# Kernel tuning notes

Measured on AMD Instinct MI355X. Metric: run time of the kernel, lower is better.

## Reference

```python
import jax, jax.numpy as jnp
import numpy as np

N_NODES = 10000
AVG_DEG = 16
N_EDGES = N_NODES * AVG_DEG
NODE_DIM, EDGE_DIM, LIN_DIM, HID, OUT, LAYERS = 9, 3, 32, 300, 2, 5


def _init(key, shape, fan_in):
    return jax.random.normal(key, shape, jnp.float32) * (1.0 / np.sqrt(fan_in))


def setup_inputs() -> dict:
    key = jax.random.key(0)
    ks = jax.random.split(key, 18)
    inp = {
        "x": jax.random.normal(ks[0], (N_NODES, NODE_DIM), jnp.float32),
        "edge_index": jax.random.randint(ks[1], (2, N_EDGES), 0, N_NODES, jnp.int32),
        "edge_attr": jax.random.normal(ks[2], (N_EDGES, EDGE_DIM), jnp.float32),
        "batch": jnp.zeros((N_NODES,), jnp.int32),
        # nn.Linear params (stored as [in, out] so fwd is x @ W + b)
        "node_w": _init(ks[3], (NODE_DIM, LIN_DIM), NODE_DIM),
        "node_b": jnp.zeros((LIN_DIM,), jnp.float32),
        "edge_w": _init(ks[4], (EDGE_DIM, LIN_DIM), EDGE_DIM),
        "edge_b": jnp.zeros((LIN_DIM,), jnp.float32),
        # GCNConv: lin (no bias) + separate additive bias (PyG convention)
        "gcn0_w": _init(ks[5], (LIN_DIM, HID), LIN_DIM),
        "gcn0_b": jnp.zeros((HID,), jnp.float32),
        "gcn_w": _init(ks[6], (LAYERS - 1, HID, HID), HID),
        "gcn_b": jnp.zeros((LAYERS - 1, HID), jnp.float32),
        "lin1_w": _init(ks[7], (HID, LIN_DIM), HID),
        "lin1_b": jnp.zeros((LIN_DIM,), jnp.float32),
        "lin2_w": _init(ks[8], (LIN_DIM, OUT), LIN_DIM),
        "lin2_b": jnp.zeros((OUT,), jnp.float32),
    }
    return inp


def reference(x, edge_index, edge_attr, batch,
              node_w, node_b, edge_w, edge_b,
              gcn0_w, gcn0_b, gcn_w, gcn_b,
              lin1_w, lin1_b, lin2_w, lin2_b):
    row, col = edge_index[0], edge_index[1]

    e = edge_attr @ edge_w + edge_b  # [E, LIN_DIM] edge embeddings

    # Faithful to the original bug: node embeddings get edge attrs scatter-added,
    # then the result is discarded by `attr = edge_attr`. Kept for fidelity (dead).
    node_h = x @ node_w + node_b
    node_h = node_h.at[row].add(e)  # unused downstream

    # GCN stack runs over the E-row edge-embedding matrix -> effective node count = E
    h = e
    n = h.shape[0]  # == N_EDGES

    # symmetric gcn_norm with self-loops (edge_weight = 1), computed once
    deg = jax.ops.segment_sum(jnp.ones((edge_index.shape[1],), h.dtype), col,
                              num_segments=n) + 1.0
    dinv = jax.lax.rsqrt(deg)
    norm = dinv[row] * dinv[col]  # per-edge normalization
    self_norm = (dinv * dinv)[:, None]  # self-loop term

    def gcn(h, w, b):
        hw = h @ w  # dense transform
        agg = jax.ops.segment_sum(hw[row] * norm[:, None], col, num_segments=n)
        return agg + self_norm * hw + b

    h = jax.nn.relu(gcn(h, gcn0_w, gcn0_b))

    def step(h, wb):
        w, b = wb
        return jax.nn.relu(gcn(h, w, b)), None

    h, _ = jax.lax.scan(step, h, (gcn_w, gcn_b))

    g = jnp.mean(h, axis=0, keepdims=True)  # [1, HID] graph readout
    g = jax.nn.relu(g @ lin1_w + lin1_b)
    pred = g @ lin2_w + lin2_b  # [1, OUT]; forward returns pre-softmax logits
    return pred
```

## Files before the change

kernel.cpp:

```cpp
#include <hip/hip_runtime.h>
#include <hip/hip_bf16.h>

#define N_NODES 10000
#define N_EDGES 160000
#define HID 300
#define HIDP 304
#define NPARTB (N_EDGES - N_NODES)
#define KS 328
#define RBM 80
#define RBF 32
#define PARTB_BLOCKS 1875
#define GEMMA_BLOCKS 125
#define FILL_BLOCKS 313
#define MEGA_BLOCKS (PARTB_BLOCKS + GEMMA_BLOCKS + FILL_BLOCKS)
#define FUSE_BLOCKS 313

typedef __attribute__((ext_vector_type(8))) short short8;
typedef __attribute__((ext_vector_type(4))) float f32x4;

#define MFMA_B16(a, b, c) __builtin_amdgcn_mfma_f32_16x16x32_bf16(a, b, c, 0, 0, 0)

__device__ __forceinline__ short bf16r(float x) {
    unsigned u = __float_as_uint(x);
    return (short)((u + 0x7fffu + ((u >> 16) & 1u)) >> 16);
}
__device__ __forceinline__ float b2f(unsigned short u) {
    return __uint_as_float(((unsigned)u) << 16);
}
__device__ __forceinline__ void split1(float x, short& hi, short& lo) {
    short h = bf16r(x);
    float hf = __uint_as_float(((unsigned)(unsigned short)h) << 16);
    hi = h;
    lo = bf16r(x - hf);
}

__global__ void k_prep(const float* __restrict__ g0w, const float* __restrict__ gw,
                       short* __restrict__ wt0, short* __restrict__ wtl,
                       const int* __restrict__ col, int* __restrict__ cnt) {
    int idx = blockIdx.x * 256 + threadIdx.x;
    if (idx < N_EDGES) atomicAdd(&cnt[col[idx]], 1);
    if (idx < 1216) {
        int n16 = idx & 15, q = (idx >> 4) & 3, nt = idx >> 6;
        int n = nt * 16 + n16;
        short* hd = wt0 + (size_t)(nt * 8 + q) * 128 + n16 * 8;
        short* ld = wt0 + (size_t)(nt * 8 + 4 + q) * 128 + n16 * 8;
#pragma unroll
        for (int j = 0; j < 8; ++j) {
            int k = q * 8 + j;
            float f = (n < HID) ? g0w[k * HID + n] : 0.0f;
            short hi, lo;
            split1(f, hi, lo);
            hd[j] = hi;
            ld[j] = lo;
        }
    } else if (idx < 1216 + 48640) {
        int i = idx - 1216;
        int n16 = i & 15; i >>= 4;
        int q = i & 3; i >>= 2;
        int nt = i % 19; i /= 19;
        int chunk = i % 10;
        int l = i / 10;
        int n = nt * 16 + n16;
        int cnt_idx = chunk * 19 + nt;
        short* base = wtl + (size_t)l * 194560;
        short* hd = base + (size_t)(cnt_idx * 8 + q) * 128 + n16 * 8;
        short* ld = base + (size_t)(cnt_idx * 8 + 4 + q) * 128 + n16 * 8;
#pragma unroll
        for (int j = 0; j < 8; ++j) {
            int k = chunk * 32 + q * 8 + j;
            float f = (k < HID && n < HID) ? gw[((size_t)l * HID + k) * HID + n] : 0.0f;
            short hi, lo;
            split1(f, hi, lo);
            hd[j] = hi;
            ld[j] = lo;
        }
    }
}

__global__ __launch_bounds__(1024) void k_scan(
    const int* __restrict__ cnt, int* __restrict__ col_start,
    int* __restrict__ cursor, float* __restrict__ dinv,
    float* __restrict__ selfnorm) {
    __shared__ int wsum[16];
    int t = threadIdx.x;
    int lane = t & 63, w = t >> 6;
    int carry = 0;
    for (int base = 0; base < N_NODES; base += 1024) {
        int i = base + t;
        int v = (i < N_NODES) ? cnt[i] : 0;
        int s = v;
#pragma unroll
        for (int d = 1; d < 64; d <<= 1) {
            int n = __shfl_up(s, d, 64);
            if (lane >= d) s += n;
        }
        if (lane == 63) wsum[w] = s;
        __syncthreads();
        int woff = 0, total = 0;
#pragma unroll
        for (int k = 0; k < 16; ++k) {
            if (k < w) woff += wsum[k];
            total += wsum[k];
        }
        if (i < N_NODES) {
            int excl = carry + woff + s - v;
            col_start[i] = excl;
            cursor[i] = excl;
            float dd = (float)v + 1.0f;
            dinv[i] = rsqrtf(dd);
            selfnorm[i] = 1.0f / dd;
        }
        carry += total;
        __syncthreads();
    }
    if (t == 0) col_start[N_NODES] = carry;
}

template <int MT, int NTC>
__device__ __forceinline__ void kloop(const short* __restrict__ wp, int nch,
                                      const short* Hh, int nt0, int quad, int l16,
                                      f32x4 (&acc)[MT][NTC]) {
#pragma unroll
    for (int mt = 0; mt < MT; ++mt)
#pragma unroll
        for (int i = 0; i < NTC; ++i)
#pragma unroll
            for (int r = 0; r < 4; ++r) acc[mt][i][r] = 0.0f;
#pragma unroll 1
    for (int c = 0; c < nch; ++c) {
        const short* cb = wp + (size_t)(c * 19 + nt0) * 1024 + quad * 128 + l16 * 8;
        short8 ah[MT];
#pragma unroll
        for (int mt = 0; mt < MT; ++mt)
            ah[mt] = *(const short8*)&Hh[(mt * 16 + l16) * KS + c * 32 + quad * 8];
        short8 bb[NTC];
#pragma unroll
        for (int i = 0; i < NTC; ++i) bb[i] = *(const short8*)(cb + (size_t)i * 1024);
#pragma unroll
        for (int mt = 0; mt < MT; ++mt)
#pragma unroll
            for (int i = 0; i < NTC; ++i)
                acc[mt][i] = MFMA_B16(ah[mt], bb[i], acc[mt][i]);
#pragma unroll
        for (int i = 0; i < NTC; ++i) bb[i] = *(const short8*)(cb + (size_t)i * 1024 + 512);
#pragma unroll
        for (int mt = 0; mt < MT; ++mt)
#pragma unroll
            for (int i = 0; i < NTC; ++i)
                acc[mt][i] = MFMA_B16(ah[mt], bb[i], acc[mt][i]);
    }
}

template <int MT, int NTC>
__device__ __forceinline__ void gcn_epilogue(const float* __restrict__ bias,
                                             int nt0, int quad, int l16,
                                             f32x4 (&acc)[MT][NTC], short* Hh) {
#pragma unroll
    for (int i = 0; i < NTC; ++i) {
        int c = (nt0 + i) * 16 + l16;
        float b = (c < HID) ? bias[c] : 0.0f;
#pragma unroll
        for (int mt = 0; mt < MT; ++mt)
#pragma unroll
            for (int r = 0; r < 4; ++r) {
                float v = fmaxf(acc[mt][i][r] + b, 0.0f);
                Hh[(mt * 16 + quad * 4 + r) * KS + c] = bf16r(v);
            }
    }
}

template <int MT, int NTC>
__device__ __forceinline__ void gcn_final(const float* __restrict__ bias,
                                          int nt0, int quad, int l16,
                                          f32x4 (&acc)[MT][NTC],
                                          float* __restrict__ gout) {
#pragma unroll
    for (int i = 0; i < NTC; ++i) {
        int c = (nt0 + i) * 16 + l16;
        float b = (c < HID) ? bias[c] : 0.0f;
        float s = 0.0f;
#pragma unroll
        for (int mt = 0; mt < MT; ++mt)
#pragma unroll
            for (int r = 0; r < 4; ++r) s += fmaxf(acc[mt][i][r] + b, 0.0f);
        s += __shfl_xor(s, 16, 64);
        s += __shfl_xor(s, 32, 64);
        if (quad == 0) gout[c] = (c < HID) ? s : 0.0f;
    }
}

template <int MT, int NTC>
__device__ __forceinline__ void gemm_out(int base, int nt0, int quad, int l16,
                                         f32x4 (&acc)[MT][NTC],
                                         unsigned short* __restrict__ HW) {
#pragma unroll
    for (int i = 0; i < NTC; ++i) {
        int c = (nt0 + i) * 16 + l16;
#pragma unroll
        for (int mt = 0; mt < MT; ++mt)
#pragma unroll
            for (int r = 0; r < 4; ++r) {
                int gm = base + mt * 16 + quad * 4 + r;
                if (gm < N_NODES)
                    HW[(size_t)gm * HIDP + c] = (unsigned short)bf16r(acc[mt][i][r]);
            }
    }
}

__global__ __launch_bounds__(512, 4) void k_mega(
    const float* __restrict__ edge_attr,
    const float* __restrict__ edge_w,
    const float* __restrict__ edge_b,
    const short* __restrict__ wt0,
    const short* __restrict__ wtl,
    const float* __restrict__ gcn0_b,
    const float* __restrict__ gcn_b,
    float* __restrict__ gpartB,
    unsigned short* __restrict__ hw0,
    const int* __restrict__ row,
    const int* __restrict__ col,
    int* __restrict__ cursor,
    const float* __restrict__ dinv,
    int2* __restrict__ edge_pack) {
    __shared__ short Hh[RBM * KS];
    int bid = blockIdx.x, t = threadIdx.x;
    int lane = t & 63, w = t >> 6;
    int l16 = lane & 15, quad = lane >> 4;
    int nt0 = (w < 3) ? w * 3 : 9 + (w - 3) * 2;

    if (bid < PARTB_BLOCKS) {
        int base = N_NODES + bid * RBM;
        for (int i = t; i < RBM * 8; i += 512) {
            int r = i >> 3, c4 = (i & 7) * 4;
            const float* ar = edge_attr + (size_t)(base + r) * 3;
            float a0 = ar[0], a1 = ar[1], a2 = ar[2];
#pragma unroll
            for (int j = 0; j < 4; ++j) {
                int cc = c4 + j;
                float v = edge_b[cc];
                v = fmaf(a0, edge_w[cc], v);
                v = fmaf(a1, edge_w[32 + cc], v);
                v = fmaf(a2, edge_w[64 + cc], v);
                Hh[r * KS + cc] = bf16r(v);
            }
        }
        for (int i = t; i < RBM * 24; i += 512) {
            int r = i / 24, k = 304 + i % 24;
            Hh[r * KS + k] = 0;
        }
        __syncthreads();

        float* gout = gpartB + (size_t)bid * HIDP;
        if (w < 3) {
            f32x4 acc[5][3];
            kloop<5, 3>(wt0, 1, Hh, nt0, quad, l16, acc);
            __syncthreads();
            gcn_epilogue<5, 3>(gcn0_b, nt0, quad, l16, acc, Hh);
            __syncthreads();
            for (int l = 0; l < 4; ++l) {
                kloop<5, 3>(wtl + (size_t)l * 194560, 10, Hh, nt0, quad, l16, acc);
                __syncthreads();
                if (l < 3) {
                    gcn_epilogue<5, 3>(gcn_b + l * HID, nt0, quad, l16, acc, Hh);
                    __syncthreads();
                } else {
                    gcn_final<5, 3>(gcn_b + l * HID, nt0, quad, l16, acc, gout);
                }
            }
        } else {
            f32x4 acc[5][2];
            kloop<5, 2>(wt0, 1, Hh, nt0, quad, l16, acc);
            __syncthreads();
            gcn_epilogue<5, 2>(gcn0_b, nt0, quad, l16, acc, Hh);
            __syncthreads();
            for (int l = 0; l < 4; ++l) {
                kloop<5, 2>(wtl + (size_t)l * 194560, 10, Hh, nt0, quad, l16, acc);
                __syncthreads();
                if (l < 3) {
                    gcn_epilogue<5, 2>(gcn_b + l * HID, nt0, quad, l16, acc, Hh);
                    __syncthreads();
                } else {
                    gcn_final<5, 2>(gcn_b + l * HID, nt0, quad, l16, acc, gout);
                }
            }
        }
    } else if (bid < PARTB_BLOCKS + GEMMA_BLOCKS) {
        int base = (bid - PARTB_BLOCKS) * RBM;
        for (int i = t; i < RBM * 8; i += 512) {
            int r = i >> 3, c4 = (i & 7) * 4;
            const float* ar = edge_attr + (size_t)(base + r) * 3;
            float a0 = ar[0], a1 = ar[1], a2 = ar[2];
#pragma unroll
            for (int j = 0; j < 4; ++j) {
                int cc = c4 + j;
                float v = edge_b[cc];
                v = fmaf(a0, edge_w[cc], v);
                v = fmaf(a1, edge_w[32 + cc], v);
                v = fmaf(a2, edge_w[64 + cc], v);
                Hh[r * KS + cc] = bf16r(v);
            }
        }
        for (int i = t; i < RBM * 24; i += 512) {
            int r = i / 24, k = 304 + i % 24;
            Hh[r * KS + k] = 0;
        }
        __syncthreads();
        if (w < 3) {
            f32x4 acc[5][3];
            kloop<5, 3>(wt0, 1, Hh, nt0, quad, l16, acc);
            gemm_out<5, 3>(base, nt0, quad, l16, acc, hw0);
        } else {
            f32x4 acc[5][2];
            kloop<5, 2>(wt0, 1, Hh, nt0, quad, l16, acc);
            gemm_out<5, 2>(base, nt0, quad, l16, acc, hw0);
        }
    } else {
        int e = (bid - PARTB_BLOCKS - GEMMA_BLOCKS) * 512 + t;
        if (e < N_EDGES) {
            int c = col[e], r = row[e];
            int p = atomicAdd(&cursor[c], 1);
            edge_pack[p] = make_int2(r, __float_as_int(dinv[r] * dinv[c]));
        }
    }
}

__device__ __forceinline__ void agg_row(int c, int lane,
                                        const unsigned short* __restrict__ hw_in,
                                        const int* __restrict__ col_start,
                                        const int2* __restrict__ edge_pack,
                                        float (&v)[5]) {
#pragma unroll
    for (int jj = 0; jj < 5; ++jj) v[jj] = 0.0f;
    int beg = col_start[c], end = col_start[c + 1];
    int i = beg;
    for (; i + 4 <= end; i += 4) {
        int2 e0 = edge_pack[i], e1 = edge_pack[i + 1];
        int2 e2 = edge_pack[i + 2], e3 = edge_pack[i + 3];
        const unsigned short* h0 = hw_in + (size_t)e0.x * HIDP;
        const unsigned short* h1 = hw_in + (size_t)e1.x * HIDP;
        const unsigned short* h2 = hw_in + (size_t)e2.x * HIDP;
        const unsigned short* h3 = hw_in + (size_t)e3.x * HIDP;
        float n0 = __int_as_float(e0.y), n1 = __int_as_float(e1.y);
        float n2 = __int_as_float(e2.y), n3 = __int_as_float(e3.y);
#pragma unroll
        for (int jj = 0; jj < 5; ++jj) {
            int cc = lane + 64 * jj;
            if (cc < HIDP) {
                float s = v[jj];
                s = fmaf(n0, b2f(h0[cc]), s);
                s = fmaf(n1, b2f(h1[cc]), s);
                s = fmaf(n2, b2f(h2[cc]), s);
                s = fmaf(n3, b2f(h3[cc]), s);
                v[jj] = s;
            }
        }
    }
    for (; i < end; ++i) {
        int2 e0 = edge_pack[i];
        const unsigned short* h0 = hw_in + (size_t)e0.x * HIDP;
        float n0 = __int_as_float(e0.y);
#pragma unroll
        for (int jj = 0; jj < 5; ++jj) {
            int cc = lane + 64 * jj;
            if (cc < HIDP) v[jj] = fmaf(n0, b2f(h0[cc]), v[jj]);
        }
    }
}

__global__ __launch_bounds__(512, 6) void k_fuse(
    const unsigned short* __restrict__ hw_in,
    const int* __restrict__ col_start,
    const int2* __restrict__ edge_pack,
    const float* __restrict__ selfnorm,
    const float* __restrict__ bias,
    const short* __restrict__ wt,
    unsigned short* __restrict__ hw_out) {
    __shared__ short Hh[RBF * KS];
    int t = threadIdx.x;
    int lane = t & 63, w = t >> 6;
    int l16 = lane & 15, quad = lane >> 4;
    int base = blockIdx.x * RBF;
    int nt0 = (w < 3) ? w * 3 : 9 + (w - 3) * 2;

#pragma unroll 1
    for (int j = 0; j < 4; ++j) {
        int r = w * 4 + j;
        int c = base + r;
        if (c < N_NODES) {
            float v[5];
            agg_row(c, lane, hw_in, col_start, edge_pack, v);
            float sn = selfnorm[c];
            const unsigned short* sp = hw_in + (size_t)c * HIDP;
#pragma unroll
            for (int jj = 0; jj < 5; ++jj) {
                int cc = lane + 64 * jj;
                if (cc < HIDP) {
                    float h = v[jj] + sn * b2f(sp[cc]) + ((cc < HID) ? bias[cc] : 0.0f);
                    Hh[r * KS + cc] = bf16r(fmaxf(h, 0.0f));
                }
            }
        } else {
#pragma unroll
            for (int jj = 0; jj < 5; ++jj) {
                int cc = lane + 64 * jj;
                if (cc < HIDP) Hh[r * KS + cc] = 0;
            }
        }
    }
    for (int i = t; i < RBF * 24; i += 512) {
        int r = i / 24, k = 304 + i % 24;
        Hh[r * KS + k] = 0;
    }
    __syncthreads();

    if (w < 3) {
        f32x4 acc[2][3];
        kloop<2, 3>(wt, 10, Hh, nt0, quad, l16, acc);
        gemm_out<2, 3>(base, nt0, quad, l16, acc, hw_out);
    } else {
        f32x4 acc[2][2];
        kloop<2, 2>(wt, 10, Hh, nt0, quad, l16, acc);
        gemm_out<2, 2>(base, nt0, quad, l16, acc, hw_out);
    }
}

__global__ __launch_bounds__(512) void k_last(
    const unsigned short* __restrict__ hw_in,
    const int* __restrict__ col_start,
    const int2* __restrict__ edge_pack,
    const float* __restrict__ selfnorm,
    const float* __restrict__ bias,
    const float* __restrict__ gpartB,
    float* __restrict__ g_sum) {
    __shared__ float red[8 * 320];
    int t = threadIdx.x;
    int lane = t & 63, w = t >> 6;
    int base = blockIdx.x * RBF;

    float s[5] = {0.0f, 0.0f, 0.0f, 0.0f, 0.0f};
#pragma unroll 1
    for (int j = 0; j < 4; ++j) {
        int c = base + w * 4 + j;
        if (c < N_NODES) {
            float v[5];
            agg_row(c, lane, hw_in, col_start, edge_pack, v);
            float sn = selfnorm[c];
            const unsigned short* sp = hw_in + (size_t)c * HIDP;
#pragma unroll
            for (int jj = 0; jj < 5; ++jj) {
                int cc = lane + 64 * jj;
                if (cc < HID) {
                    float h = v[jj] + sn * b2f(sp[cc]) + bias[cc];
                    s[jj] += fmaxf(h, 0.0f);
                }
            }
        }
    }
    if (w < 6) {
        int rr = blockIdx.x * 6 + w;
        if (rr < PARTB_BLOCKS) {
#pragma unroll
            for (int jj = 0; jj < 5; ++jj) {
                int cc = lane + 64 * jj;
                if (cc < HID) s[jj] += gpartB[(size_t)rr * HIDP + cc];
            }
        }
    }
#pragma unroll
    for (int jj = 0; jj < 5; ++jj) red[w * 320 + lane + 64 * jj] = s[jj];
    __syncthreads();
    if (w == 0) {
#pragma unroll
        for (int jj = 0; jj < 5; ++jj) {
            int cc = lane + 64 * jj;
            if (cc < HID) {
                float tot = 0.0f;
#pragma unroll
                for (int g = 0; g < 8; ++g) tot += red[g * 320 + cc];
                atomicAdd(&g_sum[cc], tot);
            }
        }
    }
}

__global__ void k_head(const float* __restrict__ g_sum,
                       const float* __restrict__ lin1_w, const float* __restrict__ lin1_b,
                       const float* __restrict__ lin2_w, const float* __restrict__ lin2_b,
                       float* __restrict__ out) {
    __shared__ float g2[32];
    int t = threadIdx.x;
    const float inv = 1.0f / (float)N_EDGES;
    if (t < 32) {
        float a = lin1_b[t];
        for (int d = 0; d < HID; ++d) a = fmaf(g_sum[d] * inv, lin1_w[d * 32 + t], a);
        g2[t] = fmaxf(a, 0.0f);
    }
    __syncthreads();
    if (t < 2) {
        float p = lin2_b[t];
        for (int j = 0; j < 32; ++j) p = fmaf(g2[j], lin2_w[j * 2 + t], p);
        out[t] = p;
    }
}


extern "C" void kernel_launch(void* const* d_in, const int* in_sizes, int n_in,
                              void* d_out, int out_size, void* d_ws, size_t ws_size,
                              hipStream_t stream) {
    (void)in_sizes; (void)n_in; (void)out_size; (void)ws_size;
    const int* edge_index = (const int*)d_in[1];
    const float* edge_attr = (const float*)d_in[2];
    const float* edge_w = (const float*)d_in[6];
    const float* edge_b = (const float*)d_in[7];
    const float* gcn0_w = (const float*)d_in[8];
    const float* gcn0_b = (const float*)d_in[9];
    const float* gcn_w = (const float*)d_in[10];
    const float* gcn_b = (const float*)d_in[11];
    const float* lin1_w = (const float*)d_in[12];
    const float* lin1_b = (const float*)d_in[13];
    const float* lin2_w = (const float*)d_in[14];
    const float* lin2_b = (const float*)d_in[15];

    char* ws = (char*)d_ws;
    size_t off = 0;
    auto alloc = [&](size_t bytes) {
        void* p = ws + off;
        off = (off + bytes + 255) & ~(size_t)255;
        return p;
    };
    unsigned short* hwA = (unsigned short*)alloc((size_t)N_NODES * HIDP * 2);
    unsigned short* hwB = (unsigned short*)alloc((size_t)N_NODES * HIDP * 2);
    int2* edge_pack = (int2*)alloc((size_t)N_EDGES * 8);
    int* cnt = (int*)alloc((size_t)N_NODES * 4);
    int* col_start = (int*)alloc((size_t)(N_NODES + 1) * 4);
    int* cursor = (int*)alloc((size_t)N_NODES * 4);
    float* dinv = (float*)alloc((size_t)N_NODES * 4);
    float* selfnorm = (float*)alloc((size_t)N_NODES * 4);
    float* g_sum = (float*)alloc((size_t)HIDP * 4);
    short* wt0 = (short*)alloc((size_t)38912);
    short* wtl = (short*)alloc((size_t)4 * 389120);
    float* gpartB = (float*)alloc((size_t)PARTB_BLOCKS * HIDP * 4);

    const int* row = edge_index;
    const int* col = edge_index + N_EDGES;

    hipMemsetAsync(cnt, 0, N_NODES * 4, stream);
    hipMemsetAsync(g_sum, 0, HIDP * 4, stream);

    k_prep<<<(N_EDGES + 255) / 256, 256, 0, stream>>>(gcn0_w, gcn_w, wt0, wtl, col, cnt);
    k_scan<<<1, 1024, 0, stream>>>(cnt, col_start, cursor, dinv, selfnorm);

    k_mega<<<MEGA_BLOCKS, 512, 0, stream>>>(edge_attr, edge_w, edge_b, wt0, wtl,
                                            gcn0_b, gcn_b, gpartB, hwA,
                                            row, col, cursor, dinv, edge_pack);

    k_fuse<<<FUSE_BLOCKS, 512, 0, stream>>>(hwA, col_start, edge_pack, selfnorm,
                                            gcn0_b, wtl + (size_t)0 * 194560, hwB);
    k_fuse<<<FUSE_BLOCKS, 512, 0, stream>>>(hwB, col_start, edge_pack, selfnorm,
                                            gcn_b + 0 * HID, wtl + (size_t)1 * 194560, hwA);
    k_fuse<<<FUSE_BLOCKS, 512, 0, stream>>>(hwA, col_start, edge_pack, selfnorm,
                                            gcn_b + 1 * HID, wtl + (size_t)2 * 194560, hwB);
    k_fuse<<<FUSE_BLOCKS, 512, 0, stream>>>(hwB, col_start, edge_pack, selfnorm,
                                            gcn_b + 2 * HID, wtl + (size_t)3 * 194560, hwA);
    k_last<<<FUSE_BLOCKS, 512, 0, stream>>>(hwA, col_start, edge_pack, selfnorm,
                                            gcn_b + 3 * HID, gpartB, g_sum);
    k_head<<<1, 64, 0, stream>>>(g_sum, lin1_w, lin1_b, lin2_w, lin2_b, (float*)d_out);
}
```

Before: 467.1 us.

## Reorder mega-kernel blocks, transpose MFMA epilogue, halve fuse tile, unroll gather by 8

Moves the edge-fill and layer-0 GEMM blocks ahead of the long part-B blocks in the mega kernel. Part-B MFMAs now use swapped operands, so each epilogue can write packed 4-wide bf16 vectors to shared memory. The fuse and last kernels process 16 rows per block instead of 32, doubling the block count, and the launch-bounds occupancy hint drops from 6 to 4. The neighbour gather adds an 8-edge unrolled loop for more memory-level parallelism. Together these aim to cut LDS store traffic and tail imbalance and to raise gather throughput, at the cost of more register pressure and more blocks that reload the weights.

```diff
diff --git a/kernel.cpp b/kernel.cpp
--- a/kernel.cpp
+++ b/kernel.cpp
@@ -8,14 +8,15 @@
 #define NPARTB (N_EDGES - N_NODES)
 #define KS 328
 #define RBM 80
-#define RBF 32
+#define RBF 16
 #define PARTB_BLOCKS 1875
 #define GEMMA_BLOCKS 125
 #define FILL_BLOCKS 313
 #define MEGA_BLOCKS (PARTB_BLOCKS + GEMMA_BLOCKS + FILL_BLOCKS)
-#define FUSE_BLOCKS 313
+#define FUSE_BLOCKS 625
 
 typedef __attribute__((ext_vector_type(8))) short short8;
+typedef __attribute__((ext_vector_type(4))) short s16x4;
 typedef __attribute__((ext_vector_type(4))) float f32x4;
 
 #define MFMA_B16(a, b, c) __builtin_amdgcn_mfma_f32_16x16x32_bf16(a, b, c, 0, 0, 0)
@@ -116,7 +117,7 @@
     if (t == 0) col_start[N_NODES] = carry;
 }
 
-template <int MT, int NTC>
+template <int MT, int NTC, bool SWAP>
 __device__ __forceinline__ void kloop(const short* __restrict__ wp, int nch,
                                       const short* Hh, int nt0, int quad, int l16,
                                       f32x4 (&acc)[MT][NTC]) {
@@ -140,52 +141,61 @@
         for (int mt = 0; mt < MT; ++mt)
 #pragma unroll
             for (int i = 0; i < NTC; ++i)
-                acc[mt][i] = MFMA_B16(ah[mt], bb[i], acc[mt][i]);
+                acc[mt][i] = SWAP ? MFMA_B16(bb[i], ah[mt], acc[mt][i])
+                                  : MFMA_B16(ah[mt], bb[i], acc[mt][i]);
 #pragma unroll
         for (int i = 0; i < NTC; ++i) bb[i] = *(const short8*)(cb + (size_t)i * 1024 + 512);
 #pragma unroll
         for (int mt = 0; mt < MT; ++mt)
 #pragma unroll
             for (int i = 0; i < NTC; ++i)
-                acc[mt][i] = MFMA_B16(ah[mt], bb[i], acc[mt][i]);
+                acc[mt][i] = SWAP ? MFMA_B16(bb[i], ah[mt], acc[mt][i])
+                                  : MFMA_B16(ah[mt], bb[i], acc[mt][i]);
     }
 }
 
 template <int MT, int NTC>
-__device__ __forceinline__ void gcn_epilogue(const float* __restrict__ bias,
-                                             int nt0, int quad, int l16,
-                                             f32x4 (&acc)[MT][NTC], short* Hh) {
+__device__ __forceinline__ void gcn_epilogueT(const float* __restrict__ bias,
+                                              int nt0, int quad, int l16,
+                                              f32x4 (&acc)[MT][NTC], short* Hh) {
 #pragma unroll
     for (int i = 0; i < NTC; ++i) {
-        int c = (nt0 + i) * 16 + l16;
-        float b = (c < HID) ? bias[c] : 0.0f;
-#pragma unroll
-        for (int mt = 0; mt < MT; ++mt)
-#pragma unroll
-            for (int r = 0; r < 4; ++r) {
-                float v = fmaxf(acc[mt][i][r] + b, 0.0f);
-                Hh[(mt * 16 + quad * 4 + r) * KS + c] = bf16r(v);
-            }
+        int f0 = (nt0 + i) * 16 + quad * 4;
+        float bv[4];
+#pragma unroll
+        for (int r = 0; r < 4; ++r) bv[r] = (f0 + r < HID) ? bias[f0 + r] : 0.0f;
+#pragma unroll
+        for (int mt = 0; mt < MT; ++mt) {
+            s16x4 pk;
+#pragma unroll
+            for (int r = 0; r < 4; ++r)
+                pk[r] = bf16r(fmaxf(acc[mt][i][r] + bv[r], 0.0f));
+            *(s16x4*)&Hh[(mt * 16 + l16) * KS + f0] = pk;
+        }
     }
 }
 
 template <int MT, int NTC>
-__device__ __forceinline__ void gcn_final(const float* __restrict__ bias,
-                                          int nt0, int quad, int l16,
-                                          f32x4 (&acc)[MT][NTC],
-                                          float* __restrict__ gout) {
+__device__ __forceinline__ void gcn_finalT(const float* __restrict__ bias,
+                                           int nt0, int quad, int l16,
+                                           f32x4 (&acc)[MT][NTC],
+                                           float* __restrict__ gout) {
 #pragma unroll
     for (int i = 0; i < NTC; ++i) {
-        int c = (nt0 + i) * 16 + l16;
-        float b = (c < HID) ? bias[c] : 0.0f;
-        float s = 0.0f;
-#pragma unroll
-        for (int mt = 0; mt < MT; ++mt)
-#pragma unroll
-            for (int r = 0; r < 4; ++r) s += fmaxf(acc[mt][i][r] + b, 0.0f);
-        s += __shfl_xor(s, 16, 64);
-        s += __shfl_xor(s, 32, 64);
-        if (quad == 0) gout[c] = (c < HID) ? s : 0.0f;
+        int f0 = (nt0 + i) * 16 + quad * 4;
+#pragma unroll
+        for (int r = 0; r < 4; ++r) {
+            int f = f0 + r;
+            float b = (f < HID) ? bias[f] : 0.0f;
+            float s = 0.0f;
+#pragma unroll
+            for (int mt = 0; mt < MT; ++mt) s += fmaxf(acc[mt][i][r] + b, 0.0f);
+            s += __shfl_xor(s, 1, 64);
+            s += __shfl_xor(s, 2, 64);
+            s += __shfl_xor(s, 4, 64);
+            s += __shfl_xor(s, 8, 64);
+            if (l16 == 0) gout[f] = (f < HID) ? s : 0.0f;
+        }
     }
 }
 
@@ -228,12 +238,20 @@
     int l16 = lane & 15, quad = lane >> 4;
     int nt0 = (w < 3) ? w * 3 : 9 + (w - 3) * 2;
 
-    if (bid < PARTB_BLOCKS) {
-        int base = N_NODES + bid * RBM;
+    if (bid < FILL_BLOCKS) {
+        int e = bid * 512 + t;
+        if (e < N_EDGES) {
+            int c = col[e], r = row[e];
+            int p = atomicAdd(&cursor[c], 1);
+            edge_pack[p] = make_int2(r, __float_as_int(dinv[r] * dinv[c]));
+        }
+    } else if (bid < FILL_BLOCKS + GEMMA_BLOCKS) {
+        int base = (bid - FILL_BLOCKS) * RBM;
         for (int i = t; i < RBM * 8; i += 512) {
             int r = i >> 3, c4 = (i & 7) * 4;
             const float* ar = edge_attr + (size_t)(base + r) * 3;
             float a0 = ar[0], a1 = ar[1], a2 = ar[2];
+            s16x4 pk;
 #pragma unroll
             for (int j = 0; j < 4; ++j) {
                 int cc = c4 + j;
@@ -241,55 +259,31 @@
                 v = fmaf(a0, edge_w[cc], v);
                 v = fmaf(a1, edge_w[32 + cc], v);
                 v = fmaf(a2, edge_w[64 + cc], v);
-                Hh[r * KS + cc] = bf16r(v);
-            }
-        }
-        for (int i = t; i < RBM * 24; i += 512) {
-            int r = i / 24, k = 304 + i % 24;
-            Hh[r * KS + k] = 0;
+                pk[j] = bf16r(v);
+            }
+            *(s16x4*)&Hh[r * KS + c4] = pk;
+        }
+        for (int i = t; i < RBM * 6; i += 512) {
+            int r = i / 6, k = 304 + (i % 6) * 4;
+            *(s16x4*)&Hh[r * KS + k] = (s16x4)0;
         }
         __syncthreads();
-
-        float* gout = gpartB + (size_t)bid * HIDP;
         if (w < 3) {
             f32x4 acc[5][3];
-            kloop<5, 3>(wt0, 1, Hh, nt0, quad, l16, acc);
-            __syncthreads();
-            gcn_epilogue<5, 3>(gcn0_b, nt0, quad, l16, acc, Hh);
-            __syncthreads();
-            for (int l = 0; l < 4; ++l) {
-                kloop<5, 3>(wtl + (size_t)l * 194560, 10, Hh, nt0, quad, l16, acc);
-                __syncthreads();
-                if (l < 3) {
-                    gcn_epilogue<5, 3>(gcn_b + l * HID, nt0, quad, l16, acc, Hh);
-                    __syncthreads();
-                } else {
-                    gcn_final<5, 3>(gcn_b + l * HID, nt0, quad, l16, acc, gout);
-                }
-            }
+            kloop<5, 3, false>(wt0, 1, Hh, nt0, quad, l16, acc);
+            gemm_out<5, 3>(base, nt0, quad, l16, acc, hw0);
         } else {
             f32x4 acc[5][2];
-            kloop<5, 2>(wt0, 1, Hh, nt0, quad, l16, acc);
-            __syncthreads();
-            gcn_epilogue<5, 2>(gcn0_b, nt0, quad, l16, acc, Hh);
-            __syncthreads();
-            for (int l = 0; l < 4; ++l) {
-                kloop<5, 2>(wtl + (size_t)l * 194560, 10, Hh, nt0, quad, l16, acc);
-                __syncthreads();
-                if (l < 3) {
-                    gcn_epilogue<5, 2>(gcn_b + l * HID, nt0, quad, l16, acc, Hh);
-                    __syncthreads();
-                } else {
-                    gcn_final<5, 2>(gcn_b + l * HID, nt0, quad, l16, acc, gout);
-                }
-            }
-        }
-    } else if (bid < PARTB_BLOCKS + GEMMA_BLOCKS) {
-        int base = (bid - PARTB_BLOCKS) * RBM;
+            kloop<5, 2, false>(wt0, 1, Hh, nt0, quad, l16, acc);
+            gemm_out<5, 2>(base, nt0, quad, l16, acc, hw0);
+        }
+    } else {
+        int base = N_NODES + (bid - FILL_BLOCKS - GEMMA_BLOCKS) * RBM;
         for (int i = t; i < RBM * 8; i += 512) {
             int r = i >> 3, c4 = (i & 7) * 4;
             const float* ar = edge_attr + (size_t)(base + r) * 3;
             float a0 = ar[0], a1 = ar[1], a2 = ar[2];
+            s16x4 pk;
 #pragma unroll
             for (int j = 0; j < 4; ++j) {
                 int cc = c4 + j;
@@ -297,29 +291,49 @@
                 v = fmaf(a0, edge_w[cc], v);
                 v = fmaf(a1, edge_w[32 + cc], v);
                 v = fmaf(a2, edge_w[64 + cc], v);
-                Hh[r * KS + cc] = bf16r(v);
-            }
-        }
-        for (int i = t; i < RBM * 24; i += 512) {
-            int r = i / 24, k = 304 + i % 24;
-            Hh[r * KS + k] = 0;
+                pk[j] = bf16r(v);
+            }
+            *(s16x4*)&Hh[r * KS + c4] = pk;
+        }
+        for (int i = t; i < RBM * 6; i += 512) {
+            int r = i / 6, k = 304 + (i % 6) * 4;
+            *(s16x4*)&Hh[r * KS + k] = (s16x4)0;
         }
         __syncthreads();
+
+        float* gout = gpartB + (size_t)(bid - FILL_BLOCKS - GEMMA_BLOCKS) * HIDP;
         if (w < 3) {
             f32x4 acc[5][3];
-            kloop<5, 3>(wt0, 1, Hh, nt0, quad, l16, acc);
-            gemm_out<5, 3>(base, nt0, quad, l16, acc, hw0);
+            kloop<5, 3, true>(wt0, 1, Hh, nt0, quad, l16, acc);
+            __syncthreads();
+            gcn_epilogueT<5, 3>(gcn0_b, nt0, quad, l16, acc, Hh);
+            __syncthreads();
+            for (int l = 0; l < 4; ++l) {
+                kloop<5, 3, true>(wtl + (size_t)l * 194560, 10, Hh, nt0, quad, l16, acc);
+                if (l < 3) {
+                    __syncthreads();
+                    gcn_epilogueT<5, 3>(gcn_b + l * HID, nt0, quad, l16, acc, Hh);
+                    __syncthreads();
+                } else {
+                    gcn_finalT<5, 3>(gcn_b + l * HID, nt0, quad, l16, acc, gout);
+                }
+            }
         } else {
             f32x4 acc[5][2];
-            kloop<5, 2>(wt0, 1, Hh, nt0, quad, l16, acc);
-            gemm_out<5, 2>(base, nt0, quad, l16, acc, hw0);
-        }
-    } else {
-        int e = (bid - PARTB_BLOCKS - GEMMA_BLOCKS) * 512 + t;
-        if (e < N_EDGES) {
-            int c = col[e], r = row[e];
-            int p = atomicAdd(&cursor[c], 1);
-            edge_pack[p] = make_int2(r, __float_as_int(dinv[r] * dinv[c]));
+            kloop<5, 2, true>(wt0, 1, Hh, nt0, quad, l16, acc);
+            __syncthreads();
+            gcn_epilogueT<5, 2>(gcn0_b, nt0, quad, l16, acc, Hh);
+            __syncthreads();
+            for (int l = 0; l < 4; ++l) {
+                kloop<5, 2, true>(wtl + (size_t)l * 194560, 10, Hh, nt0, quad, l16, acc);
+                if (l < 3) {
+                    __syncthreads();
+                    gcn_epilogueT<5, 2>(gcn_b + l * HID, nt0, quad, l16, acc, Hh);
+                    __syncthreads();
+                } else {
+                    gcn_finalT<5, 2>(gcn_b + l * HID, nt0, quad, l16, acc, gout);
+                }
+            }
         }
     }
 }
@@ -333,6 +347,42 @@
     for (int jj = 0; jj < 5; ++jj) v[jj] = 0.0f;
     int beg = col_start[c], end = col_start[c + 1];
     int i = beg;
+#pragma unroll 1
+    for (; i + 8 <= end; i += 8) {
+        int2 e0 = edge_pack[i], e1 = edge_pack[i + 1];
+        int2 e2 = edge_pack[i + 2], e3 = edge_pack[i + 3];
+        int2 e4 = edge_pack[i + 4], e5 = edge_pack[i + 5];
+        int2 e6 = edge_pack[i + 6], e7 = edge_pack[i + 7];
+        const unsigned short* h0 = hw_in + (size_t)e0.x * HIDP;
+        const unsigned short* h1 = hw_in + (size_t)e1.x * HIDP;
+        const unsigned short* h2 = hw_in + (size_t)e2.x * HIDP;
+        const unsigned short* h3 = hw_in + (size_t)e3.x * HIDP;
+        const unsigned short* h4 = hw_in + (size_t)e4.x * HIDP;
+        const unsigned short* h5 = hw_in + (size_t)e5.x * HIDP;
+        const unsigned short* h6 = hw_in + (size_t)e6.x * HIDP;
+        const unsigned short* h7 = hw_in + (size_t)e7.x * HIDP;
+        float n0 = __int_as_float(e0.y), n1 = __int_as_float(e1.y);
+        float n2 = __int_as_float(e2.y), n3 = __int_as_float(e3.y);
+        float n4 = __int_as_float(e4.y), n5 = __int_as_float(e5.y);
+        float n6 = __int_as_float(e6.y), n7 = __int_as_float(e7.y);
+#pragma unroll
+        for (int jj = 0; jj < 5; ++jj) {
+            int cc = lane + 64 * jj;
+            if (cc < HIDP) {
+                float s = v[jj];
+                s = fmaf(n0, b2f(h0[cc]), s);
+                s = fmaf(n1, b2f(h1[cc]), s);
+                s = fmaf(n2, b2f(h2[cc]), s);
+                s = fmaf(n3, b2f(h3[cc]), s);
+                s = fmaf(n4, b2f(h4[cc]), s);
+                s = fmaf(n5, b2f(h5[cc]), s);
+                s = fmaf(n6, b2f(h6[cc]), s);
+                s = fmaf(n7, b2f(h7[cc]), s);
+                v[jj] = s;
+            }
+        }
+    }
+#pragma unroll 1
     for (; i + 4 <= end; i += 4) {
         int2 e0 = edge_pack[i], e1 = edge_pack[i + 1];
         int2 e2 = edge_pack[i + 2], e3 = edge_pack[i + 3];
@@ -355,6 +405,7 @@
             }
         }
     }
+#pragma unroll 1
     for (; i < end; ++i) {
         int2 e0 = edge_pack[i];
         const unsigned short* h0 = hw_in + (size_t)e0.x * HIDP;
@@ -367,7 +418,7 @@
     }
 }
 
-__global__ __launch_bounds__(512, 6) void k_fuse(
+__global__ __launch_bounds__(512, 4) void k_fuse(
     const unsigned short* __restrict__ hw_in,
     const int* __restrict__ col_start,
     const int2* __restrict__ edge_pack,
@@ -383,44 +434,36 @@
     int nt0 = (w < 3) ? w * 3 : 9 + (w - 3) * 2;
 
 #pragma unroll 1
-    for (int j = 0; j < 4; ++j) {
-        int r = w * 4 + j;
+    for (int j = 0; j < 2; ++j) {
+        int r = w * 2 + j;
         int c = base + r;
-        if (c < N_NODES) {
-            float v[5];
-            agg_row(c, lane, hw_in, col_start, edge_pack, v);
-            float sn = selfnorm[c];
-            const unsigned short* sp = hw_in + (size_t)c * HIDP;
-#pragma unroll
-            for (int jj = 0; jj < 5; ++jj) {
-                int cc = lane + 64 * jj;
-                if (cc < HIDP) {
-                    float h = v[jj] + sn * b2f(sp[cc]) + ((cc < HID) ? bias[cc] : 0.0f);
-                    Hh[r * KS + cc] = bf16r(fmaxf(h, 0.0f));
-                }
-            }
-        } else {
-#pragma unroll
-            for (int jj = 0; jj < 5; ++jj) {
-                int cc = lane + 64 * jj;
-                if (cc < HIDP) Hh[r * KS + cc] = 0;
-            }
-        }
-    }
-    for (int i = t; i < RBF * 24; i += 512) {
-        int r = i / 24, k = 304 + i % 24;
-        Hh[r * KS + k] = 0;
+        float v[5];
+        agg_row(c, lane, hw_in, col_start, edge_pack, v);
+        float sn = selfnorm[c];
+        const unsigned short* sp = hw_in + (size_t)c * HIDP;
+#pragma unroll
+        for (int jj = 0; jj < 5; ++jj) {
+            int cc = lane + 64 * jj;
+            if (cc < HIDP) {
+                float h = v[jj] + sn * b2f(sp[cc]) + ((cc < HID) ? bias[cc] : 0.0f);
+                Hh[r * KS + cc] = bf16r(fmaxf(h, 0.0f));
+            }
+        }
+    }
+    for (int i = t; i < RBF * 6; i += 512) {
+        int r = i / 6, k = 304 + (i % 6) * 4;
+        *(s16x4*)&Hh[r * KS + k] = (s16x4)0;
     }
     __syncthreads();
 
     if (w < 3) {
-        f32x4 acc[2][3];
-        kloop<2, 3>(wt, 10, Hh, nt0, quad, l16, acc);
-        gemm_out<2, 3>(base, nt0, quad, l16, acc, hw_out);
+        f32x4 acc[1][3];
+        kloop<1, 3, false>(wt, 10, Hh, nt0, quad, l16, acc);
+        gemm_out<1, 3>(base, nt0, quad, l16, acc, hw_out);
     } else {
-        f32x4 acc[2][2];
-        kloop<2, 2>(wt, 10, Hh, nt0, quad, l16, acc);
-        gemm_out<2, 2>(base, nt0, quad, l16, acc, hw_out);
+        f32x4 acc[1][2];
+        kloop<1, 2, false>(wt, 10, Hh, nt0, quad, l16, acc);
+        gemm_out<1, 2>(base, nt0, quad, l16, acc, hw_out);
     }
 }
 
@@ -439,25 +482,23 @@
 
     float s[5] = {0.0f, 0.0f, 0.0f, 0.0f, 0.0f};
 #pragma unroll 1
-    for (int j = 0; j < 4; ++j) {
-        int c = base + w * 4 + j;
-        if (c < N_NODES) {
-            float v[5];
-            agg_row(c, lane, hw_in, col_start, edge_pack, v);
-            float sn = selfnorm[c];
-            const unsigned short* sp = hw_in + (size_t)c * HIDP;
-#pragma unroll
-            for (int jj = 0; jj < 5; ++jj) {
-                int cc = lane + 64 * jj;
-                if (cc < HID) {
-                    float h = v[jj] + sn * b2f(sp[cc]) + bias[cc];
-                    s[jj] += fmaxf(h, 0.0f);
-                }
-            }
-        }
-    }
-    if (w < 6) {
-        int rr = blockIdx.x * 6 + w;
+    for (int j = 0; j < 2; ++j) {
+        int c = base + w * 2 + j;
+        float v[5];
+        agg_row(c, lane, hw_in, col_start, edge_pack, v);
+        float sn = selfnorm[c];
+        const unsigned short* sp = hw_in + (size_t)c * HIDP;
+#pragma unroll
+        for (int jj = 0; jj < 5; ++jj) {
+            int cc = lane + 64 * jj;
+            if (cc < HID) {
+                float h = v[jj] + sn * b2f(sp[cc]) + bias[cc];
+                s[jj] += fmaxf(h, 0.0f);
+            }
+        }
+    }
+    if (w < 3) {
+        int rr = blockIdx.x * 3 + w;
         if (rr < PARTB_BLOCKS) {
 #pragma unroll
             for (int jj = 0; jj < 5; ++jj) {
```

After: 488.5 us. 1.05x slower.
